# Performance work log

Measured on AMD Instinct MI355X. Metric: run time of the kernel, lower is better.

## Reference

```python
import jax, jax.numpy as jnp
import numpy as np

N = 50000      # nodes
E = 400000     # edges
D_IN = 128
D = 256        # d_hidden
H = 8          # heads
C = D // H     # head dim (PyG out_channels)
L = 3          # layers
SCALE = 1.0 / np.sqrt(C).astype(np.float32)


def setup_inputs() -> dict:
    key = jax.random.key(0)
    ks = jax.random.split(key, 16)
    w = lambda k, shape: (jax.random.normal(k, shape, jnp.float32) * 0.02)
    inp = {
        "x": jax.random.normal(ks[0], (N, D_IN), jnp.float32),
        "edge_index": jax.random.randint(ks[1], (2, E), 0, N, dtype=jnp.int64),
        # input projection
        "W_in": w(ks[2], (D, D_IN)), "b_in": jnp.zeros((D,), jnp.float32),
        # stacked TransformerConv params: query/key/value/skip linears per layer
        "Wq": w(ks[3], (L, D, D)), "bq": jnp.zeros((L, D), jnp.float32),
        "Wk": w(ks[4], (L, D, D)), "bk": jnp.zeros((L, D), jnp.float32),
        "Wv": w(ks[5], (L, D, D)), "bv": jnp.zeros((L, D), jnp.float32),
        "Ws": w(ks[6], (L, D, D)), "bs": jnp.zeros((L, D), jnp.float32),
        # layer norms
        "ln_g": jnp.ones((L, D), jnp.float32), "ln_b": jnp.zeros((L, D), jnp.float32),
        # edge classifier: Linear(2D,D) -> ReLU -> Linear(D,1)
        "Wec1": w(ks[7], (D, 2 * D)), "bec1": jnp.zeros((D,), jnp.float32),
        "Wec2": w(ks[8], (1, D)), "bec2": jnp.zeros((1,), jnp.float32),
        # param predictor: Linear(2D,D) -> ReLU -> Linear(D,2) -> softplus
        "Wpp1": w(ks[9], (D, 2 * D)), "bpp1": jnp.zeros((D,), jnp.float32),
        "Wpp2": w(ks[10], (2, D)), "bpp2": jnp.zeros((2,), jnp.float32),
    }
    return inp


def _layer_norm(h, g, b):
    mu = jnp.mean(h, axis=-1, keepdims=True)
    var = jnp.mean(jnp.square(h - mu), axis=-1, keepdims=True)
    return (h - mu) * jax.lax.rsqrt(var + 1e-5) * g + b


def _transformer_conv(h, src, dst, Wq, bq, Wk, bk, Wv, bv, Ws, bs):
    # PyG TransformerConv (concat=True, root_weight=True, eval mode / no dropout)
    q = (h @ Wq.T + bq).reshape(N, H, C)
    k = (h @ Wk.T + bk).reshape(N, H, C)
    v = (h @ Wv.T + bv).reshape(N, H, C)
    # per-edge attention logits: query at dst, key at src  -> [E, H]
    alpha = jnp.einsum('ehc,ehc->eh', q[dst], k[src]) * SCALE
    # scatter-softmax over incoming edges of each dst node
    amax = jax.lax.stop_gradient(jax.ops.segment_max(alpha, dst, num_segments=N))
    ea = jnp.exp(alpha - amax[dst])
    denom = jax.ops.segment_sum(ea, dst, num_segments=N)
    a = ea / (denom[dst] + 1e-16)
    # weighted scatter-add of values  -> [N, H, C] -> [N, D]
    out = jax.ops.segment_sum(a[:, :, None] * v[src], dst, num_segments=N).reshape(N, D)
    return out + h @ Ws.T + bs  # skip connection (lin_skip)


def reference(x, edge_index, W_in, b_in, Wq, bq, Wk, bk, Wv, bv, Ws, bs,
              ln_g, ln_b, Wec1, bec1, Wec2, bec2, Wpp1, bpp1, Wpp2, bpp2):
    src, dst = edge_index[0], edge_index[1]
    h = x @ W_in.T + b_in
    for l in range(L):
        h_new = _transformer_conv(h, src, dst, Wq[l], bq[l], Wk[l], bk[l],
                                  Wv[l], bv[l], Ws[l], bs[l])
        h = _layer_norm(h + h_new, ln_g[l], ln_b[l])
    # per-edge features [E, 2D]
    ef = jnp.concatenate([h[src], h[dst]], axis=1)
    he = jax.nn.relu(ef @ Wec1.T + bec1)
    edge_logits = (he @ Wec2.T + bec2).squeeze(-1)
    hp = jax.nn.relu(ef @ Wpp1.T + bpp1)
    edge_params = jax.nn.softplus(hp @ Wpp2.T + bpp2)
    return edge_logits, edge_params
```

## Files before the change

kernel.cpp:

```cpp
#include <hip/hip_runtime.h>
#include <math.h>

typedef __bf16 bf16_t;
typedef __attribute__((ext_vector_type(8))) __bf16 bf16x8;
typedef __attribute__((ext_vector_type(4))) __bf16 bf16x4;
typedef __attribute__((ext_vector_type(4))) float f32x4;

#define MFMA16(a,b,c) __builtin_amdgcn_mfma_f32_16x16x32_bf16((a),(b),(c),0,0,0)

__device__ __forceinline__ void gload_lds16(const bf16_t* g, bf16_t* l) {
  __builtin_amdgcn_global_load_lds(
      (const __attribute__((address_space(1))) unsigned int*)g,
      (__attribute__((address_space(3))) unsigned int*)l, 16, 0, 0);
}

__global__ __launch_bounds__(256) void k_cvt4(const float* __restrict__ x,
                                              bf16_t* __restrict__ o, int n4) {
  int i = blockIdx.x * 256 + threadIdx.x;
  if (i >= n4) return;
  f32x4 v = *(const f32x4*)(x + (size_t)i * 4);
  bf16x4 b;
  b[0] = (bf16_t)v[0]; b[1] = (bf16_t)v[1]; b[2] = (bf16_t)v[2]; b[3] = (bf16_t)v[3];
  *(bf16x4*)(o + (size_t)i * 4) = b;
}

__global__ __launch_bounds__(256) void k_prep_w(
    const float* __restrict__ W_in,
    const float* __restrict__ Wq, const float* __restrict__ Wk,
    const float* __restrict__ Wv, const float* __restrict__ Ws,
    const float* __restrict__ bq, const float* __restrict__ bk,
    const float* __restrict__ bv, const float* __restrict__ bs,
    const float* __restrict__ Wec1, const float* __restrict__ Wpp1,
    const float* __restrict__ bec1, const float* __restrict__ bpp1,
    bf16_t* __restrict__ w_in_b, bf16_t* __restrict__ wqkvs_b,
    float* __restrict__ bqkvs, bf16_t* __restrict__ wnode_b,
    float* __restrict__ bnode) {
  int i = blockIdx.x * 256 + threadIdx.x;
  const int S0 = 256 * 128, S1 = 3 * 1024 * 256, S2 = 1024 * 256, S3 = 3 * 1024, S4 = 1024;
  if (i < S0) { w_in_b[i] = (bf16_t)W_in[i]; return; }
  i -= S0;
  if (i < S1) {
    int l = i / (1024 * 256), rem = i % (1024 * 256);
    int row = rem >> 8, col = rem & 255;
    const float* srcp = (row < 256) ? Wq : (row < 512) ? Wk : (row < 768) ? Wv : Ws;
    wqkvs_b[i] = (bf16_t)srcp[((size_t)l * 256 + (row & 255)) * 256 + col];
    return;
  }
  i -= S1;
  if (i < S2) {
    int row = i >> 8, col = i & 255;
    float v;
    if (row < 256)       v = Wec1[row * 512 + col];
    else if (row < 512)  v = Wec1[(row - 256) * 512 + 256 + col];
    else if (row < 768)  v = Wpp1[(row - 512) * 512 + col];
    else                 v = Wpp1[(row - 768) * 512 + 256 + col];
    wnode_b[i] = (bf16_t)v;
    return;
  }
  i -= S2;
  if (i < S3) {
    int l = i >> 10, row = i & 1023;
    const float* srcp = (row < 256) ? bq : (row < 512) ? bk : (row < 768) ? bv : bs;
    bqkvs[i] = srcp[l * 256 + (row & 255)];
    return;
  }
  i -= S3;
  if (i < S4) {
    bnode[i] = (i < 256) ? bec1[i] : ((i >= 512 && i < 768) ? bpp1[i - 512] : 0.f);
  }
}

__global__ __launch_bounds__(256) void k_gemm128(
    const bf16_t* __restrict__ A, const bf16_t* __restrict__ W,
    const float* __restrict__ bias, float* __restrict__ Cf,
    bf16_t* __restrict__ Cb, int M, int N, int K) {
  __shared__ bf16_t As[2][128 * 32];
  __shared__ bf16_t Bs[2][128 * 32];
  const int t = threadIdx.x;
  const int lane = t & 63, wave = t >> 6;
  const int wm = wave >> 1, wn = wave & 1;
  const int mi = lane & 15, ks = lane >> 4;
  const int bm = blockIdx.x * 128, bn = blockIdx.y * 128;
  const int scol = (lane & 3) * 8;
  int ra0 = bm + wave * 32 + (lane >> 2);
  int ra1 = ra0 + 16;
  ra0 = (ra0 < M) ? ra0 : (M - 1);
  ra1 = (ra1 < M) ? ra1 : (M - 1);
  const int rb0 = bn + wave * 32 + (lane >> 2);
  const int rb1 = rb0 + 16;

  auto stage = [&](int buf, int k0) {
    gload_lds16(A + (size_t)ra0 * K + k0 + scol, &As[buf][(wave * 32) * 32]);
    gload_lds16(A + (size_t)ra1 * K + k0 + scol, &As[buf][(wave * 32 + 16) * 32]);
    gload_lds16(W + (size_t)rb0 * K + k0 + scol, &Bs[buf][(wave * 32) * 32]);
    gload_lds16(W + (size_t)rb1 * K + k0 + scol, &Bs[buf][(wave * 32 + 16) * 32]);
  };

  f32x4 acc[4][4];
#pragma unroll
  for (int i = 0; i < 4; i++)
#pragma unroll
    for (int j = 0; j < 4; j++) acc[i][j] = (f32x4){0.f, 0.f, 0.f, 0.f};

  stage(0, 0);
  __syncthreads();
  const int nk = K >> 5;
  int cur = 0;
  for (int kt = 0; kt < nk; ++kt) {
    if (kt + 1 < nk) stage(cur ^ 1, (kt + 1) << 5);
    bf16x8 af[4], bf[4];
#pragma unroll
    for (int i = 0; i < 4; i++)
      af[i] = *(const bf16x8*)&As[cur][(wm * 64 + i * 16 + mi) * 32 + ks * 8];
#pragma unroll
    for (int j = 0; j < 4; j++)
      bf[j] = *(const bf16x8*)&Bs[cur][(wn * 64 + j * 16 + mi) * 32 + ks * 8];
#pragma unroll
    for (int i = 0; i < 4; i++)
#pragma unroll
      for (int j = 0; j < 4; j++) acc[i][j] = MFMA16(bf[j], af[i], acc[i][j]);
    __syncthreads();
    cur ^= 1;
  }
#pragma unroll
  for (int i = 0; i < 4; i++) {
    int gm = bm + wm * 64 + i * 16 + mi;
    if (gm >= M) continue;
    size_t rowb = (size_t)gm * N;
#pragma unroll
    for (int j = 0; j < 4; j++) {
      int gn = bn + wn * 64 + j * 16 + ks * 4;
      f32x4 v = acc[i][j];
      if (bias) v = v + *(const f32x4*)(bias + gn);
      if (Cf) *(f32x4*)(Cf + rowb + gn) = v;
      if (Cb) {
        bf16x4 vb;
        vb[0] = (bf16_t)v[0]; vb[1] = (bf16_t)v[1];
        vb[2] = (bf16_t)v[2]; vb[3] = (bf16_t)v[3];
        *(bf16x4*)(Cb + rowb + gn) = vb;
      }
    }
  }
}

__global__ __launch_bounds__(256) void k_count(const int* __restrict__ dstv,
                                               int* __restrict__ counts, int E) {
  int e = blockIdx.x * 256 + threadIdx.x;
  if (e < E) atomicAdd(&counts[dstv[e]], 1);
}

__global__ __launch_bounds__(256) void k_scan_a(const int* __restrict__ counts,
                                                int* __restrict__ pre,
                                                int* __restrict__ blk, int n) {
  const int t = threadIdx.x;
  const int gid = blockIdx.x * 256 + t;
  const int lane = t & 63, wv = t >> 6;
  int c = (gid < n) ? counts[gid] : 0;
  int v = c;
#pragma unroll
  for (int off = 1; off < 64; off <<= 1) {
    int u = __shfl_up(v, off);
    if (lane >= off) v += u;
  }
  __shared__ int wsum[4];
  if (lane == 63) wsum[wv] = v;
  __syncthreads();
  if (t == 0) {
    int s = 0;
#pragma unroll
    for (int i = 0; i < 4; i++) { int x = wsum[i]; wsum[i] = s; s += x; }
  }
  __syncthreads();
  int excl = v - c + wsum[wv];
  if (gid < n) pre[gid] = excl;
  if (t == 255) blk[blockIdx.x] = excl + c;
}

__global__ __launch_bounds__(256) void k_scan_b(int* __restrict__ blk, int nb) {
  const int t = threadIdx.x;
  const int lane = t & 63, wv = t >> 6;
  int c = (t < nb) ? blk[t] : 0;
  int v = c;
#pragma unroll
  for (int off = 1; off < 64; off <<= 1) {
    int u = __shfl_up(v, off);
    if (lane >= off) v += u;
  }
  __shared__ int wsum[4];
  if (lane == 63) wsum[wv] = v;
  __syncthreads();
  if (t == 0) {
    int s = 0;
#pragma unroll
    for (int i = 0; i < 4; i++) { int x = wsum[i]; wsum[i] = s; s += x; }
  }
  __syncthreads();
  if (t < nb) blk[t] = v - c + wsum[wv];
}

__global__ __launch_bounds__(256) void k_scan_c(const int* __restrict__ counts,
                                                const int* __restrict__ pre,
                                                const int* __restrict__ blk,
                                                int* __restrict__ row_ptr,
                                                int* __restrict__ cursor, int n) {
  const int gid = blockIdx.x * 256 + threadIdx.x;
  if (gid >= n) return;
  int excl = blk[blockIdx.x] + pre[gid];
  cursor[gid] = excl;
  row_ptr[gid + 1] = excl + counts[gid];
  if (gid == 0) row_ptr[0] = 0;
}

__global__ __launch_bounds__(256) void k_fill(const int* __restrict__ srcv,
                                              const int* __restrict__ dstv,
                                              int* __restrict__ cursor,
                                              int* __restrict__ csr_src,
                                              int* __restrict__ csr_dst,
                                              int* __restrict__ csr_eid, int E) {
  int e = blockIdx.x * 256 + threadIdx.x;
  if (e < E) {
    int d = dstv[e];
    int slot = atomicAdd(&cursor[d], 1);
    csr_src[slot] = srcv[e];
    csr_dst[slot] = d;
    csr_eid[slot] = e;
  }
}

__global__ __launch_bounds__(256) void k_attn_ln(
    const bf16_t* __restrict__ qkvs, const int* __restrict__ row_ptr,
    const int* __restrict__ csr_src, float* __restrict__ hf,
    bf16_t* __restrict__ hb, const float* __restrict__ g,
    const float* __restrict__ b, int Nn) {
  const int lane = threadIdx.x & 63, wave = threadIdx.x >> 6;
  const int n = blockIdx.x * 4 + wave;
  if (n >= Nn) return;
  const float SC = 0.17677669529663688f;
  bf16x4 qv = *(const bf16x4*)(qkvs + (size_t)n * 1024 + lane * 4);
  float q0 = (float)qv[0] * SC, q1 = (float)qv[1] * SC;
  float q2 = (float)qv[2] * SC, q3 = (float)qv[3] * SC;
  float m[4], ls[4], a0[4], a1[4], a2[4], a3[4];
#pragma unroll
  for (int j = 0; j < 4; j++) {
    m[j] = -INFINITY; ls[j] = 0.f; a0[j] = 0.f; a1[j] = 0.f; a2[j] = 0.f; a3[j] = 0.f;
  }
  const int beg = row_ptr[n], end = row_ptr[n + 1];
  int idx = beg;
  for (; idx + 4 <= end; idx += 4) {
    int s[4];
    bf16x4 kv[4], vv[4];
#pragma unroll
    for (int j = 0; j < 4; j++) s[j] = csr_src[idx + j];
#pragma unroll
    for (int j = 0; j < 4; j++) {
      const bf16_t* base = qkvs + (size_t)s[j] * 1024;
      kv[j] = *(const bf16x4*)(base + 256 + lane * 4);
      vv[j] = *(const bf16x4*)(base + 512 + lane * 4);
    }
    float d[4];
#pragma unroll
    for (int j = 0; j < 4; j++)
      d[j] = q0 * (float)kv[j][0] + q1 * (float)kv[j][1] +
             q2 * (float)kv[j][2] + q3 * (float)kv[j][3];
#pragma unroll
    for (int j = 0; j < 4; j++) d[j] += __shfl_xor(d[j], 1);
#pragma unroll
    for (int j = 0; j < 4; j++) d[j] += __shfl_xor(d[j], 2);
#pragma unroll
    for (int j = 0; j < 4; j++) d[j] += __shfl_xor(d[j], 4);
#pragma unroll
    for (int j = 0; j < 4; j++) {
      float mn = fmaxf(m[j], d[j]);
      float sc = __expf(m[j] - mn);
      float p = __expf(d[j] - mn);
      ls[j] = ls[j] * sc + p;
      a0[j] = a0[j] * sc + p * (float)vv[j][0];
      a1[j] = a1[j] * sc + p * (float)vv[j][1];
      a2[j] = a2[j] * sc + p * (float)vv[j][2];
      a3[j] = a3[j] * sc + p * (float)vv[j][3];
      m[j] = mn;
    }
  }
  for (; idx < end; ++idx) {
    int s0 = csr_src[idx];
    const bf16_t* base = qkvs + (size_t)s0 * 1024;
    bf16x4 kv = *(const bf16x4*)(base + 256 + lane * 4);
    bf16x4 vv = *(const bf16x4*)(base + 512 + lane * 4);
    float d = q0 * (float)kv[0] + q1 * (float)kv[1] + q2 * (float)kv[2] + q3 * (float)kv[3];
    d += __shfl_xor(d, 1);
    d += __shfl_xor(d, 2);
    d += __shfl_xor(d, 4);
    float mn = fmaxf(m[0], d);
    float sc = __expf(m[0] - mn);
    float p = __expf(d - mn);
    ls[0] = ls[0] * sc + p;
    a0[0] = a0[0] * sc + p * (float)vv[0];
    a1[0] = a1[0] * sc + p * (float)vv[1];
    a2[0] = a2[0] * sc + p * (float)vv[2];
    a3[0] = a3[0] * sc + p * (float)vv[3];
    m[0] = mn;
  }
#pragma unroll
  for (int step = 0; step < 3; ++step) {
    int dst = (step == 2) ? 0 : step;
    int src = (step == 2) ? 1 : step + 2;
    float mn = fmaxf(m[dst], m[src]);
    float sD = (m[dst] == mn) ? 1.f : __expf(m[dst] - mn);
    float sS = (m[src] == mn) ? 1.f : __expf(m[src] - mn);
    ls[dst] = ls[dst] * sD + ls[src] * sS;
    a0[dst] = a0[dst] * sD + a0[src] * sS;
    a1[dst] = a1[dst] * sD + a1[src] * sS;
    a2[dst] = a2[dst] * sD + a2[src] * sS;
    a3[dst] = a3[dst] * sD + a3[src] * sS;
    m[dst] = mn;
  }
  float inv = 1.f / (ls[0] + 1e-16f);
  const int c = lane * 4;
  f32x4 hv = *(const f32x4*)(hf + (size_t)n * 256 + c);
  bf16x4 sv = *(const bf16x4*)(qkvs + (size_t)n * 1024 + 768 + c);
  float x0 = hv[0] + a0[0] * inv + (float)sv[0];
  float x1 = hv[1] + a1[0] * inv + (float)sv[1];
  float x2 = hv[2] + a2[0] * inv + (float)sv[2];
  float x3 = hv[3] + a3[0] * inv + (float)sv[3];
  float sum = x0 + x1 + x2 + x3;
  float sq = x0 * x0 + x1 * x1 + x2 * x2 + x3 * x3;
#pragma unroll
  for (int mm = 1; mm < 64; mm <<= 1) {
    sum += __shfl_xor(sum, mm);
    sq += __shfl_xor(sq, mm);
  }
  float mu = sum * (1.f / 256.f);
  float var = sq * (1.f / 256.f) - mu * mu;
  float rs = rsqrtf(var + 1e-5f);
  f32x4 y;
  y[0] = (x0 - mu) * rs * g[c] + b[c];
  y[1] = (x1 - mu) * rs * g[c + 1] + b[c + 1];
  y[2] = (x2 - mu) * rs * g[c + 2] + b[c + 2];
  y[3] = (x3 - mu) * rs * g[c + 3] + b[c + 3];
  *(f32x4*)(hf + (size_t)n * 256 + c) = y;
  bf16x4 yb;
  yb[0] = (bf16_t)y[0]; yb[1] = (bf16_t)y[1]; yb[2] = (bf16_t)y[2]; yb[3] = (bf16_t)y[3];
  *(bf16x4*)(hb + (size_t)n * 256 + c) = yb;
}

#define EF_SLOTS 8
__device__ __forceinline__ f32x4 cvt_lo(bf16x8 v) {
  bf16x4 h = __builtin_shufflevector(v, v, 0, 1, 2, 3);
  return __builtin_convertvector(h, f32x4);
}
__device__ __forceinline__ f32x4 cvt_hi(bf16x8 v) {
  bf16x4 h = __builtin_shufflevector(v, v, 4, 5, 6, 7);
  return __builtin_convertvector(h, f32x4);
}
__global__ __launch_bounds__(256) void k_edge_final(
    const bf16_t* __restrict__ Pb, const int* __restrict__ csr_src,
    const int* __restrict__ csr_dst, const int* __restrict__ csr_eid,
    const float* __restrict__ wec2, const float* __restrict__ wpp2,
    const float* __restrict__ bec2, const float* __restrict__ bpp2,
    float* __restrict__ out, int E) {
  const int t = threadIdx.x;
  const int sub = t & 15;
  const int grp = blockIdx.x * 16 + (t >> 4);
  const int slot0 = grp * EF_SLOTS;
  if (slot0 >= E) return;
  const int slot1 = (slot0 + EF_SLOTS < E) ? slot0 + EF_SLOTS : E;
  f32x4 w_ec[2][2], w_p0[2][2], w_p1[2][2];
#pragma unroll
  for (int h = 0; h < 2; h++) {
    int cb = h * 128 + sub * 8;
    w_ec[h][0] = *(const f32x4*)(wec2 + cb);
    w_ec[h][1] = *(const f32x4*)(wec2 + cb + 4);
    w_p0[h][0] = *(const f32x4*)(wpp2 + cb);
    w_p0[h][1] = *(const f32x4*)(wpp2 + cb + 4);
    w_p1[h][0] = *(const f32x4*)(wpp2 + 256 + cb);
    w_p1[h][1] = *(const f32x4*)(wpp2 + 256 + cb + 4);
  }
  const float be = bec2[0], bp0 = bpp2[0], bp1 = bpp2[1];
  const f32x4 zero = (f32x4){0.f, 0.f, 0.f, 0.f};
  int cur_dst = -1;
  f32x4 eR[2][2], pR[2][2];
  for (int slot = slot0; slot < slot1; ++slot) {
    int dn = csr_dst[slot];
    if (dn != cur_dst) {
      cur_dst = dn;
      const bf16_t* pd = Pb + (size_t)dn * 1024;
#pragma unroll
      for (int h = 0; h < 2; h++) {
        int cb = h * 128 + sub * 8;
        bf16x8 a = *(const bf16x8*)(pd + 256 + cb);
        bf16x8 p = *(const bf16x8*)(pd + 768 + cb);
        eR[h][0] = cvt_lo(a);
        eR[h][1] = cvt_hi(a);
        pR[h][0] = cvt_lo(p);
        pR[h][1] = cvt_hi(p);
      }
    }
    const bf16_t* ps = Pb + (size_t)csr_src[slot] * 1024;
    f32x4 v0 = zero, v1 = zero, v2 = zero;
#pragma unroll
    for (int h = 0; h < 2; h++) {
      int cb = h * 128 + sub * 8;
      bf16x8 eL = *(const bf16x8*)(ps + cb);
      bf16x8 pL = *(const bf16x8*)(ps + 512 + cb);
      f32x4 el0 = cvt_lo(eL), el1 = cvt_hi(eL);
      f32x4 pl0 = cvt_lo(pL), pl1 = cvt_hi(pL);
      f32x4 he0 = __builtin_elementwise_max(el0 + eR[h][0], zero);
      f32x4 he1 = __builtin_elementwise_max(el1 + eR[h][1], zero);
      f32x4 hp0 = __builtin_elementwise_max(pl0 + pR[h][0], zero);
      f32x4 hp1 = __builtin_elementwise_max(pl1 + pR[h][1], zero);
      v0 += he0 * w_ec[h][0] + he1 * w_ec[h][1];
      v1 += hp0 * w_p0[h][0] + hp1 * w_p0[h][1];
      v2 += hp0 * w_p1[h][0] + hp1 * w_p1[h][1];
    }
    float s0 = v0[0] + v0[1] + v0[2] + v0[3];
    float s1 = v1[0] + v1[1] + v1[2] + v1[3];
    float s2 = v2[0] + v2[1] + v2[2] + v2[3];
#pragma unroll
    for (int mm = 1; mm < 16; mm <<= 1) {
      s0 += __shfl_xor(s0, mm);
      s1 += __shfl_xor(s1, mm);
      s2 += __shfl_xor(s2, mm);
    }
    if (sub == 0) {
      int eid = csr_eid[slot];
      out[eid] = s0 + be;
      float p0 = s1 + bp0;
      float p1 = s2 + bp1;
      out[(size_t)E + 2 * eid]     = fmaxf(p0, 0.f) + log1pf(__expf(-fabsf(p0)));
      out[(size_t)E + 2 * eid + 1] = fmaxf(p1, 0.f) + log1pf(__expf(-fabsf(p1)));
    }
  }
}

extern "C" void kernel_launch(void* const* d_in, const int* in_sizes, int n_in,
                              void* d_out, int out_size, void* d_ws, size_t ws_size,
                              hipStream_t stream) {
  const float* x    = (const float*)d_in[0];
  const int*   ei   = (const int*)d_in[1];
  const float* W_in = (const float*)d_in[2];
  const float* b_in = (const float*)d_in[3];
  const float* Wq   = (const float*)d_in[4];
  const float* bq   = (const float*)d_in[5];
  const float* Wk   = (const float*)d_in[6];
  const float* bk   = (const float*)d_in[7];
  const float* Wv   = (const float*)d_in[8];
  const float* bv   = (const float*)d_in[9];
  const float* Ws   = (const float*)d_in[10];
  const float* bs   = (const float*)d_in[11];
  const float* ln_g = (const float*)d_in[12];
  const float* ln_b = (const float*)d_in[13];
  const float* Wec1 = (const float*)d_in[14];
  const float* bec1 = (const float*)d_in[15];
  const float* Wec2 = (const float*)d_in[16];
  const float* bec2 = (const float*)d_in[17];
  const float* Wpp1 = (const float*)d_in[18];
  const float* bpp1 = (const float*)d_in[19];
  const float* Wpp2 = (const float*)d_in[20];
  const float* bpp2 = (const float*)d_in[21];

  const int N = in_sizes[0] / 128;
  const int E = in_sizes[1] / 2;
  const int* srcv = ei;
  const int* dstv = ei + E;
  const int NB = (N + 255) / 256;

  char* w = (char*)d_ws;
  size_t off = 0;
  auto carve = [&](size_t bytes) -> char* {
    char* p = w + off;
    off = (off + bytes + 255) & ~(size_t)255;
    return p;
  };
  bf16_t* xb      = (bf16_t*)carve((size_t)N * 128 * 2);
  bf16_t* hb      = (bf16_t*)carve((size_t)N * 256 * 2);
  float*  hf      = (float*) carve((size_t)N * 256 * 4);
  bf16_t* qkvsb   = (bf16_t*)carve((size_t)N * 1024 * 2);
  bf16_t* w_in_b  = (bf16_t*)carve((size_t)256 * 128 * 2);
  bf16_t* wqkvs_b = (bf16_t*)carve((size_t)3 * 1024 * 256 * 2);
  float*  bqkvs   = (float*) carve((size_t)3 * 1024 * 4);
  bf16_t* wnode_b = (bf16_t*)carve((size_t)1024 * 256 * 2);
  float*  bnode   = (float*) carve((size_t)1024 * 4);
  int*    counts  = (int*)   carve((size_t)N * 4);
  int*    row_ptr = (int*)   carve((size_t)(N + 1) * 4);
  int*    cursor  = (int*)   carve((size_t)N * 4);
  int*    pre     = (int*)   carve((size_t)N * 4);
  int*    blk     = (int*)   carve((size_t)256 * 4);
  int*    csr_src = (int*)   carve((size_t)E * 4);
  int*    csr_dst = (int*)   carve((size_t)E * 4);
  int*    csr_eid = (int*)   carve((size_t)E * 4);

  hipMemsetAsync(counts, 0, (size_t)N * 4, stream);

  int n4 = N * 128 / 4;
  k_cvt4<<<dim3((n4 + 255) / 256), dim3(256), 0, stream>>>(x, xb, n4);
  const int PREP_TOT = 256 * 128 + 3 * 1024 * 256 + 1024 * 256 + 3 * 1024 + 1024;
  k_prep_w<<<dim3((PREP_TOT + 255) / 256), dim3(256), 0, stream>>>(
      W_in, Wq, Wk, Wv, Ws, bq, bk, bv, bs, Wec1, Wpp1, bec1, bpp1,
      w_in_b, wqkvs_b, bqkvs, wnode_b, bnode);

  k_gemm128<<<dim3((N + 127) / 128, 2), dim3(256), 0, stream>>>(
      xb, w_in_b, b_in, hf, hb, N, 256, 128);

  k_count<<<dim3((E + 255) / 256), dim3(256), 0, stream>>>(dstv, counts, E);
  k_scan_a<<<dim3(NB), dim3(256), 0, stream>>>(counts, pre, blk, N);
  k_scan_b<<<dim3(1), dim3(256), 0, stream>>>(blk, NB);
  k_scan_c<<<dim3(NB), dim3(256), 0, stream>>>(counts, pre, blk, row_ptr, cursor, N);
  k_fill<<<dim3((E + 255) / 256), dim3(256), 0, stream>>>(
      srcv, dstv, cursor, csr_src, csr_dst, csr_eid, E);

  for (int l = 0; l < 3; ++l) {
    k_gemm128<<<dim3((N + 127) / 128, 8), dim3(256), 0, stream>>>(
        hb, wqkvs_b + (size_t)l * 1024 * 256, bqkvs + l * 1024,
        (float*)nullptr, qkvsb, N, 1024, 256);
    k_attn_ln<<<dim3((N + 3) / 4), dim3(256), 0, stream>>>(
        qkvsb, row_ptr, csr_src, hf, hb, ln_g + l * 256, ln_b + l * 256, N);
  }

  k_gemm128<<<dim3((N + 127) / 128, 8), dim3(256), 0, stream>>>(
      hb, wnode_b, bnode, (float*)nullptr, qkvsb, N, 1024, 256);
  int ngroups = (E + EF_SLOTS - 1) / EF_SLOTS;
  k_edge_final<<<dim3((ngroups + 15) / 16), dim3(256), 0, stream>>>(
      qkvsb, csr_src, csr_dst, csr_eid, Wec2, Wpp2, bec2, bpp2, (float*)d_out, E);
}
```

Baseline: 837.1 us.

## Widen GEMM tile to 128x256 and drop fp32 hidden-state copy

The GEMM kernel now computes 128x256 output tiles with twice the accumulators per wave, halving the number of column blocks and the re-reading of the A operand. The fp32 copy of the hidden state is removed, so the residual in attention+layernorm is read from the bf16 buffer and only bf16 is written back. This is meant to cut global memory traffic per layer. In exchange the residual path loses precision, and register and LDS use per block rise.

```diff
diff --git a/kernel.cpp b/kernel.cpp
--- a/kernel.cpp
+++ b/kernel.cpp
@@ -70,37 +70,39 @@
   }
 }
 
-__global__ __launch_bounds__(256) void k_gemm128(
+__global__ __launch_bounds__(256) void k_gemm256(
     const bf16_t* __restrict__ A, const bf16_t* __restrict__ W,
-    const float* __restrict__ bias, float* __restrict__ Cf,
-    bf16_t* __restrict__ Cb, int M, int N, int K) {
+    const float* __restrict__ bias, bf16_t* __restrict__ Cb,
+    int M, int N, int K) {
   __shared__ bf16_t As[2][128 * 32];
-  __shared__ bf16_t Bs[2][128 * 32];
+  __shared__ bf16_t Bs[2][256 * 32];
   const int t = threadIdx.x;
   const int lane = t & 63, wave = t >> 6;
   const int wm = wave >> 1, wn = wave & 1;
   const int mi = lane & 15, ks = lane >> 4;
-  const int bm = blockIdx.x * 128, bn = blockIdx.y * 128;
+  const int bm = blockIdx.x * 128, bn = blockIdx.y * 256;
+  const int srow = lane >> 2;
   const int scol = (lane & 3) * 8;
-  int ra0 = bm + wave * 32 + (lane >> 2);
+  int ra0 = bm + wave * 32 + srow;
   int ra1 = ra0 + 16;
   ra0 = (ra0 < M) ? ra0 : (M - 1);
   ra1 = (ra1 < M) ? ra1 : (M - 1);
-  const int rb0 = bn + wave * 32 + (lane >> 2);
-  const int rb1 = rb0 + 16;
+  const int rb = bn + wave * 64 + srow;
 
   auto stage = [&](int buf, int k0) {
     gload_lds16(A + (size_t)ra0 * K + k0 + scol, &As[buf][(wave * 32) * 32]);
     gload_lds16(A + (size_t)ra1 * K + k0 + scol, &As[buf][(wave * 32 + 16) * 32]);
-    gload_lds16(W + (size_t)rb0 * K + k0 + scol, &Bs[buf][(wave * 32) * 32]);
-    gload_lds16(W + (size_t)rb1 * K + k0 + scol, &Bs[buf][(wave * 32 + 16) * 32]);
+    gload_lds16(W + (size_t)rb * K + k0 + scol,        &Bs[buf][(wave * 64) * 32]);
+    gload_lds16(W + (size_t)(rb + 16) * K + k0 + scol, &Bs[buf][(wave * 64 + 16) * 32]);
+    gload_lds16(W + (size_t)(rb + 32) * K + k0 + scol, &Bs[buf][(wave * 64 + 32) * 32]);
+    gload_lds16(W + (size_t)(rb + 48) * K + k0 + scol, &Bs[buf][(wave * 64 + 48) * 32]);
   };
 
-  f32x4 acc[4][4];
+  f32x4 acc[4][8];
 #pragma unroll
   for (int i = 0; i < 4; i++)
 #pragma unroll
-    for (int j = 0; j < 4; j++) acc[i][j] = (f32x4){0.f, 0.f, 0.f, 0.f};
+    for (int j = 0; j < 8; j++) acc[i][j] = (f32x4){0.f, 0.f, 0.f, 0.f};
 
   stage(0, 0);
   __syncthreads();
@@ -108,17 +110,17 @@
   int cur = 0;
   for (int kt = 0; kt < nk; ++kt) {
     if (kt + 1 < nk) stage(cur ^ 1, (kt + 1) << 5);
-    bf16x8 af[4], bf[4];
+    bf16x8 af[4], bfr[8];
 #pragma unroll
     for (int i = 0; i < 4; i++)
       af[i] = *(const bf16x8*)&As[cur][(wm * 64 + i * 16 + mi) * 32 + ks * 8];
 #pragma unroll
-    for (int j = 0; j < 4; j++)
-      bf[j] = *(const bf16x8*)&Bs[cur][(wn * 64 + j * 16 + mi) * 32 + ks * 8];
+    for (int j = 0; j < 8; j++)
+      bfr[j] = *(const bf16x8*)&Bs[cur][(wn * 128 + j * 16 + mi) * 32 + ks * 8];
 #pragma unroll
     for (int i = 0; i < 4; i++)
 #pragma unroll
-      for (int j = 0; j < 4; j++) acc[i][j] = MFMA16(bf[j], af[i], acc[i][j]);
+      for (int j = 0; j < 8; j++) acc[i][j] = MFMA16(bfr[j], af[i], acc[i][j]);
     __syncthreads();
     cur ^= 1;
   }
@@ -128,17 +130,13 @@
     if (gm >= M) continue;
     size_t rowb = (size_t)gm * N;
 #pragma unroll
-    for (int j = 0; j < 4; j++) {
-      int gn = bn + wn * 64 + j * 16 + ks * 4;
-      f32x4 v = acc[i][j];
-      if (bias) v = v + *(const f32x4*)(bias + gn);
-      if (Cf) *(f32x4*)(Cf + rowb + gn) = v;
-      if (Cb) {
-        bf16x4 vb;
-        vb[0] = (bf16_t)v[0]; vb[1] = (bf16_t)v[1];
-        vb[2] = (bf16_t)v[2]; vb[3] = (bf16_t)v[3];
-        *(bf16x4*)(Cb + rowb + gn) = vb;
-      }
+    for (int j = 0; j < 8; j++) {
+      int gn = bn + wn * 128 + j * 16 + ks * 4;
+      f32x4 v = acc[i][j] + *(const f32x4*)(bias + gn);
+      bf16x4 vb;
+      vb[0] = (bf16_t)v[0]; vb[1] = (bf16_t)v[1];
+      vb[2] = (bf16_t)v[2]; vb[3] = (bf16_t)v[3];
+      *(bf16x4*)(Cb + rowb + gn) = vb;
     }
   }
 }
@@ -229,9 +227,8 @@
 
 __global__ __launch_bounds__(256) void k_attn_ln(
     const bf16_t* __restrict__ qkvs, const int* __restrict__ row_ptr,
-    const int* __restrict__ csr_src, float* __restrict__ hf,
-    bf16_t* __restrict__ hb, const float* __restrict__ g,
-    const float* __restrict__ b, int Nn) {
+    const int* __restrict__ csr_src, bf16_t* __restrict__ hb,
+    const float* __restrict__ g, const float* __restrict__ b, int Nn) {
   const int lane = threadIdx.x & 63, wave = threadIdx.x >> 6;
   const int n = blockIdx.x * 4 + wave;
   if (n >= Nn) return;
@@ -316,12 +313,12 @@
   }
   float inv = 1.f / (ls[0] + 1e-16f);
   const int c = lane * 4;
-  f32x4 hv = *(const f32x4*)(hf + (size_t)n * 256 + c);
+  bf16x4 hv = *(const bf16x4*)(hb + (size_t)n * 256 + c);
   bf16x4 sv = *(const bf16x4*)(qkvs + (size_t)n * 1024 + 768 + c);
-  float x0 = hv[0] + a0[0] * inv + (float)sv[0];
-  float x1 = hv[1] + a1[0] * inv + (float)sv[1];
-  float x2 = hv[2] + a2[0] * inv + (float)sv[2];
-  float x3 = hv[3] + a3[0] * inv + (float)sv[3];
+  float x0 = (float)hv[0] + a0[0] * inv + (float)sv[0];
+  float x1 = (float)hv[1] + a1[0] * inv + (float)sv[1];
+  float x2 = (float)hv[2] + a2[0] * inv + (float)sv[2];
+  float x3 = (float)hv[3] + a3[0] * inv + (float)sv[3];
   float sum = x0 + x1 + x2 + x3;
   float sq = x0 * x0 + x1 * x1 + x2 * x2 + x3 * x3;
 #pragma unroll
@@ -337,7 +334,6 @@
   y[1] = (x1 - mu) * rs * g[c + 1] + b[c + 1];
   y[2] = (x2 - mu) * rs * g[c + 2] + b[c + 2];
   y[3] = (x3 - mu) * rs * g[c + 3] + b[c + 3];
-  *(f32x4*)(hf + (size_t)n * 256 + c) = y;
   bf16x4 yb;
   yb[0] = (bf16_t)y[0]; yb[1] = (bf16_t)y[1]; yb[2] = (bf16_t)y[2]; yb[3] = (bf16_t)y[3];
   *(bf16x4*)(hb + (size_t)n * 256 + c) = yb;
@@ -473,7 +469,6 @@
   };
   bf16_t* xb      = (bf16_t*)carve((size_t)N * 128 * 2);
   bf16_t* hb      = (bf16_t*)carve((size_t)N * 256 * 2);
-  float*  hf      = (float*) carve((size_t)N * 256 * 4);
   bf16_t* qkvsb   = (bf16_t*)carve((size_t)N * 1024 * 2);
   bf16_t* w_in_b  = (bf16_t*)carve((size_t)256 * 128 * 2);
   bf16_t* wqkvs_b = (bf16_t*)carve((size_t)3 * 1024 * 256 * 2);
@@ -498,8 +493,8 @@
       W_in, Wq, Wk, Wv, Ws, bq, bk, bv, bs, Wec1, Wpp1, bec1, bpp1,
       w_in_b, wqkvs_b, bqkvs, wnode_b, bnode);
 
-  k_gemm128<<<dim3((N + 127) / 128, 2), dim3(256), 0, stream>>>(
-      xb, w_in_b, b_in, hf, hb, N, 256, 128);
+  k_gemm256<<<dim3((N + 127) / 128, 1), dim3(256), 0, stream>>>(
+      xb, w_in_b, b_in, hb, N, 256, 128);
 
   k_count<<<dim3((E + 255) / 256), dim3(256), 0, stream>>>(dstv, counts, E);
   k_scan_a<<<dim3(NB), dim3(256), 0, stream>>>(counts, pre, blk, N);
@@ -509,15 +504,14 @@
       srcv, dstv, cursor, csr_src, csr_dst, csr_eid, E);
 
   for (int l = 0; l < 3; ++l) {
-    k_gemm128<<<dim3((N + 127) / 128, 8), dim3(256), 0, stream>>>(
-        hb, wqkvs_b + (size_t)l * 1024 * 256, bqkvs + l * 1024,
-        (float*)nullptr, qkvsb, N, 1024, 256);
+    k_gemm256<<<dim3((N + 127) / 128, 4), dim3(256), 0, stream>>>(
+        hb, wqkvs_b + (size_t)l * 1024 * 256, bqkvs + l * 1024, qkvsb, N, 1024, 256);
     k_attn_ln<<<dim3((N + 3) / 4), dim3(256), 0, stream>>>(
-        qkvsb, row_ptr, csr_src, hf, hb, ln_g + l * 256, ln_b + l * 256, N);
-  }
-
-  k_gemm128<<<dim3((N + 127) / 128, 8), dim3(256), 0, stream>>>(
-      hb, wnode_b, bnode, (float*)nullptr, qkvsb, N, 1024, 256);
+        qkvsb, row_ptr, csr_src, hb, ln_g + l * 256, ln_b + l * 256, N);
+  }
+
+  k_gemm256<<<dim3((N + 127) / 128, 4), dim3(256), 0, stream>>>(
+      hb, wnode_b, bnode, qkvsb, N, 1024, 256);
   int ngroups = (E + EF_SLOTS - 1) / EF_SLOTS;
   k_edge_final<<<dim3((ngroups + 15) / 16), dim3(256), 0, stream>>>(
       qkvsb, csr_src, csr_dst, csr_eid, Wec2, Wpp2, bec2, bpp2, (float*)d_out, E);
```

After: 885.7 us. 1.06x slower.
